# Performance work log

Hardware: AMD Instinct MI355X
Metric: run time of the kernel (lower is better)

The kernel has to match this reference:

```python
import jax, jax.numpy as jnp
import numpy as np

N, Q, CC = 8, 300, 92          # batch, queries, logit channels (91 classes + 1 objectness)
CF, HF, WF = 2048, 42, 42      # backbone feature map
M, TOPK = 20, 5                # GT boxes per image, pseudo-unknown top-k
NUM_CLASSES = 91
L_CLS, L_IOU, L_L1 = 2.0, 2.0, 5.0
NEG = -1e11


def cxcywh_to_xyxy(bx):
    cx, cy, bw, bh = bx[..., 0], bx[..., 1], bx[..., 2], bx[..., 3]
    return jnp.stack([cx - bw / 2, cy - bh / 2, cx + bw / 2, cy + bh / 2], -1)


def setup_inputs() -> dict:
    key = jax.random.key(0)
    ks = jax.random.split(key, 6)
    h = w = 1333
    img_features = jax.random.normal(ks[0], (N, CF, HF, WF), jnp.float32)
    pred_logits = jax.random.normal(ks[1], (N, Q, CC), jnp.float32)
    pred_boxes = jax.random.uniform(ks[2], (N, Q, 4), jnp.float32, 0.05, 0.95)
    tgt_labels = jax.random.randint(ks[3], (N, M), 0, NUM_CLASSES - 1).astype(jnp.int32)
    u = jax.random.uniform(ks[4], (N, M, 4), jnp.float32)
    # GT boxes in pixel cxcywh (bbox_normalize divides by image size)
    tgt_boxes = jnp.stack([u[..., 0] * w, u[..., 1] * h,
                           u[..., 2] * 0.3 * w + 2.0, u[..., 3] * 0.3 * h + 2.0], -1)
    perm = jax.vmap(lambda k: jax.random.permutation(k, Q))(jax.random.split(ks[5], N))
    query_idx = perm[:, :M].astype(jnp.int32)          # unique matched query per target
    tgt_idx = jnp.tile(jnp.arange(M, dtype=jnp.int32), (N, 1))
    return dict(img_features=img_features, pred_logits=pred_logits, pred_boxes=pred_boxes,
                tgt_labels=tgt_labels, tgt_boxes=tgt_boxes, query_idx=query_idx,
                tgt_idx=tgt_idx, h=h, w=w)


def _loss(img_features, pred_logits, pred_boxes, tgt_boxes, tgt_labels, query_idx, tgt_idx, h, w):
    b = jnp.arange(N)[:, None]
    scale = jnp.array([w, h, w, h], jnp.float32)
    out_prob = jnp.concatenate([jax.nn.softmax(pred_logits[..., :-1], -1),
                                jax.nn.sigmoid(pred_logits[..., -1:])], -1)  # [N,Q,92]
    matched_mask = jnp.zeros((N, Q), bool).at[b, query_idx].set(True)

    # --- per-query crop-mean pooling: bilinear upsample once + summed-area table ---
    mean_feat = jnp.mean(img_features, 1)                                  # [N,HF,WF]
    up = jax.vmap(lambda f: jax.image.resize(f, (h, w), 'bilinear'))(mean_feat)  # [N,h,w]
    sat = jnp.pad(jnp.cumsum(jnp.cumsum(up, 1), 2), ((0, 0), (1, 0), (1, 0)))    # [N,h+1,w+1]
    bb = cxcywh_to_xyxy(pred_boxes) * scale                                # pixel xyxy
    x1 = jnp.clip(bb[..., 0].astype(jnp.int32), 0, w)
    y1 = jnp.clip(bb[..., 1].astype(jnp.int32), 0, h)
    x2 = jnp.clip(bb[..., 2].astype(jnp.int32), 0, w)
    y2 = jnp.clip(bb[..., 3].astype(jnp.int32), 0, h)
    cnt = jnp.maximum(y2 - y1, 0) * jnp.maximum(x2 - x1, 0)
    x2e, y2e = jnp.maximum(x2, x1), jnp.maximum(y2, y1)
    boxsum = sat[b, y2e, x2e] - sat[b, y1, x2e] - sat[b, y2e, x1] + sat[b, y1, x1]
    means = jnp.where(cnt > 0, boxsum / jnp.maximum(cnt, 1), NEG)          # empty crop -> -1e11 (nan case)
    means = jnp.where(matched_mask, NEG, means)                            # matched queries excluded
    _, topk_idx = jax.lax.top_k(means, TOPK)                               # [N,TOPK]
    topk_mask = jnp.zeros((N, Q), bool).at[b, topk_idx].set(True)

    # --- matched terms ---
    tgt_cls = tgt_labels[b, tgt_idx]                                       # [N,M]
    tgt_bb = tgt_boxes[b, tgt_idx] / scale                                 # bbox_normalize
    q_cls = out_prob[b, query_idx, :NUM_CLASSES]                           # probs; CE re-applies log_softmax (faithful)
    q_obj = out_prob[b, query_idx, -1]
    q_bb = pred_boxes[b, query_idx]
    logp = jax.nn.log_softmax(q_cls, -1)
    ce_matched = -jnp.mean(jnp.take_along_axis(logp, tgt_cls[..., None].astype(jnp.int32), -1)[..., 0], 1)
    bce_matched = -jnp.mean(jnp.maximum(jnp.log(q_obj), -100.0), 1)
    l1 = jnp.sqrt(jnp.sum((q_bb - tgt_bb) ** 2, (1, 2)))                   # torch.dist (Frobenius)
    a, t = cxcywh_to_xyxy(q_bb), cxcywh_to_xyxy(tgt_bb)
    ix1 = jnp.maximum(a[..., 0], t[..., 0]); iy1 = jnp.maximum(a[..., 1], t[..., 1])
    ix2 = jnp.minimum(a[..., 2], t[..., 2]); iy2 = jnp.minimum(a[..., 3], t[..., 3])
    inter = jnp.clip(ix2 - ix1, 0.0) * jnp.clip(iy2 - iy1, 0.0)
    area = lambda z: (z[..., 2] - z[..., 0]) * (z[..., 3] - z[..., 1])
    iou = inter / (area(a) + area(t) - inter + 1e-9)
    iou_loss = jnp.sum(1.0 - iou, 1)

    # --- pseudo-unknown terms ---
    pk_cls = out_prob[b, topk_idx, :NUM_CLASSES]
    ce_pseudo = -jnp.mean(jax.nn.log_softmax(pk_cls, -1)[..., NUM_CLASSES - 1], 1)
    pk_obj = out_prob[b, topk_idx, -1]
    bce_topk = -jnp.mean(jnp.maximum(jnp.log(pk_obj), -100.0), 1)
    rest = (~matched_mask) & (~topk_mask)                                  # setdiff(other, topk)
    neglog1m = -jnp.maximum(jnp.log1p(-out_prob[..., -1]), -100.0)
    bce_rest = jnp.sum(jnp.where(rest, neglog1m, 0.0), 1) / jnp.maximum(jnp.sum(rest, 1), 1)

    cls_loss = jnp.sum(ce_matched + ce_pseudo)
    obj_loss = jnp.sum(bce_matched + bce_rest + bce_topk)
    return (cls_loss * L_CLS + obj_loss * L_CLS
            + jnp.sum(iou_loss) * L_IOU + jnp.sum(l1) * L_L1)


def reference(img_features, pred_logits, pred_boxes, tgt_labels, tgt_boxes, query_idx, tgt_idx, h, w):
    return _loss(img_features, pred_logits, pred_boxes, tgt_boxes, tgt_labels, query_idx, tgt_idx, h, w)
```

## Files before the change

### kernel.cpp

```cpp
#include <hip/hip_runtime.h>
#include <math.h>

#define NB 8
#define QN 300
#define CCH 92
#define NCLS 91
#define CFCH 2048
#define HFD 42
#define MT 20
#define TOPK5 5
#define DIM 1333
#define DIMF 1333.0f
#define PIX (HFD*HFD)
#define PIX4 (PIX/4)
#define CHUNKS 64
#define CPC (CFCH/CHUNKS)
#define NEGV -100000000000.0f

#define PART_BLOCKS (NB*CHUNKS*2)
#define CUM_TOTAL   (2*(DIM+1)*HFD)
#define CUM_BLOCKS  ((CUM_TOTAL + 255)/256)

__device__ __forceinline__ float bilin_w(int i, int j, float s) {
    float sf = ((float)i + 0.5f) * s - 0.5f;
    if (sf <= 0.f)                return (j == 0) ? 1.f : 0.f;
    if (sf >= (float)(HFD - 1))   return (j == HFD - 1) ? 1.f : 0.f;
    int j0 = (int)sf;
    float fr = sf - (float)j0;
    if (j == j0)     return 1.f - fr;
    if (j == j0 + 1) return fr;
    return 0.f;
}

__device__ __forceinline__ float wave_sum(float v) {
    for (int off = 32; off; off >>= 1) v += __shfl_down(v, off);
    return v;
}

__global__ __launch_bounds__(256) void stage_a(const float4* __restrict__ img,
                                               float4* __restrict__ part,
                                               float* __restrict__ CX,
                                               float* __restrict__ CY,
                                               float* __restrict__ out) {
    int blk = blockIdx.x;
    if (blk == 0 && threadIdx.x == 0) out[0] = 0.f;
    if (blk < PART_BLOCKS) {
        int tile = blk & 1;
        int chunk = (blk >> 1) & (CHUNKS - 1);
        int b = blk >> 7;
        int f = tile * 256 + threadIdx.x;
        if (f >= PIX4) return;
        const float4* p = img + (size_t)(b * CFCH + chunk * CPC) * PIX4 + f;
        float x = 0.f, y = 0.f, z = 0.f, w = 0.f;
#pragma unroll 8
        for (int k = 0; k < CPC; ++k) {
            float4 v = p[(size_t)k * PIX4];
            x += v.x; y += v.y; z += v.z; w += v.w;
        }
        float4 o; o.x = x; o.y = y; o.z = z; o.w = w;
        part[(size_t)(blk >> 1) * PIX4 + f] = o;
    } else {
        int idx = (blk - PART_BLOCKS) * 256 + threadIdx.x;
        const int total = (DIM + 1) * HFD;
        int t = idx / total;
        if (t >= 2) return;
        int rem = idx - t * total;
        int X = rem / HFD;
        int j = rem - X * HFD;
        const float s = (float)HFD / DIMF;
        int i0 = max(0, (int)floorf(((float)j - 0.5f) / s - 0.5f) - 2);
        int i1 = min(DIM, (int)ceilf(((float)j + 1.5f) / s - 0.5f) + 2);
        int hi = min(X, i1);
        float acc = 0.f;
        for (int i = i0; i < hi; ++i) acc += bilin_w(i, j, s);
        float* C = t ? CY : CX;
        C[X * HFD + j] = acc;
    }
}

__global__ __launch_bounds__(256) void chan_reduce(const float* __restrict__ part,
                                                   float* __restrict__ mf) {
    int idx = blockIdx.x * 256 + threadIdx.x;
    if (idx >= NB * PIX) return;
    int b = idx / PIX, pix = idx - b * PIX;
    const float* pp = part + (size_t)b * CHUNKS * PIX + pix;
    float acc = 0.f;
#pragma unroll 8
    for (int c = 0; c < CHUNKS; ++c) acc += pp[(size_t)c * PIX];
    mf[idx] = acc * (1.0f / (float)CFCH);
}

__global__ __launch_bounds__(256) void query_stats(
        const float* __restrict__ boxes, const int* __restrict__ query_idx,
        const int* __restrict__ tgt_idx, const int* __restrict__ tgt_labels,
        const float* __restrict__ tgt_boxes, const float* __restrict__ mf,
        const float* __restrict__ CX, const float* __restrict__ CY,
        const float* __restrict__ logits,
        float* __restrict__ means, float* __restrict__ ls2a,
        float* __restrict__ p90a, float* __restrict__ ptga,
        float* __restrict__ nobja, float* __restrict__ n1ma,
        float* __restrict__ l1a, float* __restrict__ ioua) {
    int gw = (blockIdx.x * 256 + threadIdx.x) >> 6;
    int lane = threadIdx.x & 63;
    if (gw >= NB * QN) return;
    int b = gw / QN, q = gw - b * QN;

    int mpos = -1;
#pragma unroll
    for (int m = 0; m < MT; ++m) if (query_idx[b * MT + m] == q) mpos = m;

    const float* bx = boxes + (size_t)gw * 4;
    float cx = bx[0], cy = bx[1], bw = bx[2], bh = bx[3];
    int x1 = min(max((int)((cx - bw * 0.5f) * DIMF), 0), DIM);
    int y1 = min(max((int)((cy - bh * 0.5f) * DIMF), 0), DIM);
    int x2 = min(max((int)((cx + bw * 0.5f) * DIMF), 0), DIM);
    int y2 = min(max((int)((cy + bh * 0.5f) * DIMF), 0), DIM);
    int x2e = max(x2, x1), y2e = max(y2, y1);
    int cnt = max(y2 - y1, 0) * max(x2 - x1, 0);
    float val = NEGV;
    if (mpos < 0 && cnt > 0) {
        float dxl = 0.f, dyl = 0.f;
        if (lane < HFD) {
            dxl = CX[x2e * HFD + lane] - CX[x1 * HFD + lane];
            dyl = CY[y2e * HFD + lane] - CY[y1 * HFD + lane];
        }
        float tacc = 0.f;
        if (lane < HFD) {
            const float* mb = mf + (size_t)b * PIX + lane;
            float inner = 0.f;
#pragma unroll 7
            for (int p = 0; p < HFD; ++p)
                inner += __shfl(dyl, p) * mb[p * HFD];
            tacc = dxl * inner;
        }
        tacc = wave_sum(tacc);
        val = tacc / (float)cnt;
    }

    const float* L = logits + (size_t)gw * CCH;
    float c0 = L[lane];
    float e1 = (lane < CCH - 64) ? L[lane + 64] : 0.f;
    bool has_c1 = (lane < NCLS - 64);
    float mx = fmaxf(c0, has_c1 ? e1 : -3.4e38f);
    for (int off = 32; off; off >>= 1) mx = fmaxf(mx, __shfl_xor(mx, off));
    float se = expf(c0 - mx) + (has_c1 ? expf(e1 - mx) : 0.f);
    for (int off = 32; off; off >>= 1) se += __shfl_xor(se, off);
    float inv = 1.f / se;
    float s2 = expf(expf(c0 - mx) * inv) + (has_c1 ? expf(expf(e1 - mx) * inv) : 0.f);
    for (int off = 32; off; off >>= 1) s2 += __shfl_xor(s2, off);
    float ls2 = logf(s2);
    float l90  = __shfl(e1, 26);
    float lobj = __shfl(e1, 27);
    float p90 = expf(l90 - mx) * inv;
    float sg = 1.f / (1.f + expf(-lobj));
    float nobj = -fmaxf(logf(sg), -100.f);
    float n1m  = -fmaxf(log1pf(-sg), -100.f);

    float ptg = 0.f, l1 = 0.f, iouc = 0.f;
    if (mpos >= 0) {
        int ti = tgt_idx[b * MT + mpos];
        int tc = tgt_labels[b * MT + ti];
        ptg = expf(L[tc] - mx) * inv;
        const float* tb = tgt_boxes + (size_t)(b * MT + ti) * 4;
        float t0 = tb[0] / DIMF, t1 = tb[1] / DIMF, t2 = tb[2] / DIMF, t3 = tb[3] / DIMF;
        float d0 = cx - t0, d1 = cy - t1, d2 = bw - t2, d3 = bh - t3;
        l1 = d0 * d0 + d1 * d1 + d2 * d2 + d3 * d3;
        float ax1 = cx - bw * 0.5f, ay1 = cy - bh * 0.5f;
        float ax2 = cx + bw * 0.5f, ay2 = cy + bh * 0.5f;
        float tx1 = t0 - t2 * 0.5f, ty1 = t1 - t3 * 0.5f;
        float tx2 = t0 + t2 * 0.5f, ty2 = t1 + t3 * 0.5f;
        float ix1 = fmaxf(ax1, tx1), iy1 = fmaxf(ay1, ty1);
        float ix2 = fminf(ax2, tx2), iy2 = fminf(ay2, ty2);
        float inter = fmaxf(ix2 - ix1, 0.f) * fmaxf(iy2 - iy1, 0.f);
        float aa = (ax2 - ax1) * (ay2 - ay1), at = (tx2 - tx1) * (ty2 - ty1);
        float iou = inter / (aa + at - inter + 1e-9f);
        iouc = 1.f - iou;
    }
    if (lane == 0) {
        means[gw] = val; ls2a[gw] = ls2; p90a[gw] = p90; ptga[gw] = ptg;
        nobja[gw] = nobj; n1ma[gw] = n1m; l1a[gw] = l1; ioua[gw] = iouc;
    }
}

__global__ __launch_bounds__(256) void finalize(
        const int* __restrict__ query_idx,
        const float* __restrict__ means, const float* __restrict__ ls2a,
        const float* __restrict__ p90a, const float* __restrict__ ptga,
        const float* __restrict__ nobja, const float* __restrict__ n1ma,
        const float* __restrict__ l1a, const float* __restrict__ ioua,
        float* __restrict__ out) {
    int b = blockIdx.x, tid = threadIdx.x;
    int wid = tid >> 6, lane = tid & 63;
    __shared__ float s_means[QN];
    __shared__ unsigned char s_matched[QN], s_sel[QN];
    __shared__ float s_red[4];
    __shared__ int s_redi[4];
    __shared__ float s_acc[4][8];

    for (int q = tid; q < QN; q += 256) {
        s_means[q] = means[b * QN + q];
        s_matched[q] = 0; s_sel[q] = 0;
    }
    __syncthreads();
    if (tid < MT) s_matched[query_idx[b * MT + tid]] = 1;
    __syncthreads();

    for (int r = 0; r < TOPK5; ++r) {
        float bv = -3.4e38f; int bi = QN;
        for (int q = tid; q < QN; q += 256) {
            if (!s_sel[q]) {
                float v = s_means[q];
                if (v > bv || (v == bv && q < bi)) { bv = v; bi = q; }
            }
        }
        for (int off = 32; off; off >>= 1) {
            float ov = __shfl_down(bv, off); int oi = __shfl_down(bi, off);
            if (ov > bv || (ov == bv && oi < bi)) { bv = ov; bi = oi; }
        }
        if (lane == 0) { s_red[wid] = bv; s_redi[wid] = bi; }
        __syncthreads();
        if (tid == 0) {
            float fv = s_red[0]; int fi = s_redi[0];
            for (int k = 1; k < 4; ++k)
                if (s_red[k] > fv || (s_red[k] == fv && s_redi[k] < fi)) { fv = s_red[k]; fi = s_redi[k]; }
            s_sel[fi] = 1;
        }
        __syncthreads();
    }

    float a0 = 0, a1 = 0, a2 = 0, a3 = 0, a4 = 0, a5 = 0, a6 = 0; int rc = 0;
    for (int q = tid; q < QN; q += 256) {
        int g = b * QN + q;
        if (s_matched[q]) {
            a0 += ls2a[g] - ptga[g];
            a1 += nobja[g];
            a2 += l1a[g];
            a3 += ioua[g];
        } else if (s_sel[q]) {
            a4 += ls2a[g] - p90a[g];
            a5 += nobja[g];
        } else {
            a6 += n1ma[g]; rc++;
        }
    }
    a0 = wave_sum(a0); a1 = wave_sum(a1); a2 = wave_sum(a2); a3 = wave_sum(a3);
    a4 = wave_sum(a4); a5 = wave_sum(a5); a6 = wave_sum(a6);
    float rcf = wave_sum((float)rc);
    if (lane == 0) {
        s_acc[wid][0] = a0; s_acc[wid][1] = a1; s_acc[wid][2] = a2; s_acc[wid][3] = a3;
        s_acc[wid][4] = a4; s_acc[wid][5] = a5; s_acc[wid][6] = a6; s_acc[wid][7] = rcf;
    }
    __syncthreads();
    if (tid == 0) {
        float A[8];
        for (int k = 0; k < 8; ++k)
            A[k] = s_acc[0][k] + s_acc[1][k] + s_acc[2][k] + s_acc[3][k];
        float ce_matched = A[0] / (float)MT;
        float bce_matched = A[1] / (float)MT;
        float l1 = sqrtf(A[2]);
        float iou_loss = A[3];
        float ce_pseudo = A[4] / (float)TOPK5;
        float bce_topk = A[5] / (float)TOPK5;
        int rcT = (int)(A[7] + 0.5f);
        float bce_rest = A[6] / (float)max(rcT, 1);
        float total = 2.f * (ce_matched + ce_pseudo)
                    + 2.f * (bce_matched + bce_rest + bce_topk)
                    + 2.f * iou_loss + 5.f * l1;
        atomicAdd(out, total);
    }
}

extern "C" void kernel_launch(void* const* d_in, const int* in_sizes, int n_in,
                              void* d_out, int out_size, void* d_ws, size_t ws_size,
                              hipStream_t stream) {
    const float* img        = (const float*)d_in[0];
    const float* logits     = (const float*)d_in[1];
    const float* boxes      = (const float*)d_in[2];
    const int*   tgt_labels = (const int*)d_in[3];
    const float* tgt_boxes  = (const float*)d_in[4];
    const int*   query_idx  = (const int*)d_in[5];
    const int*   tgt_idx    = (const int*)d_in[6];

    float* ws    = (float*)d_ws;
    float* part  = ws;
    float* mf    = part + (size_t)NB * CHUNKS * PIX;
    float* CX    = mf + (size_t)NB * PIX;
    float* CY    = CX + (size_t)(DIM + 1) * HFD;
    float* means = CY + (size_t)(DIM + 1) * HFD;
    float* ls2a  = means + NB * QN;
    float* p90a  = ls2a + NB * QN;
    float* ptga  = p90a + NB * QN;
    float* nobja = ptga + NB * QN;
    float* n1ma  = nobja + NB * QN;
    float* l1a   = n1ma + NB * QN;
    float* ioua  = l1a + NB * QN;

    stage_a<<<PART_BLOCKS + CUM_BLOCKS, 256, 0, stream>>>(
        (const float4*)img, (float4*)part, CX, CY, (float*)d_out);
    chan_reduce<<<(NB * PIX + 255) / 256, 256, 0, stream>>>(part, mf);
    query_stats<<<(NB * QN) / 4, 256, 0, stream>>>(
        boxes, query_idx, tgt_idx, tgt_labels, tgt_boxes, mf, CX, CY, logits,
        means, ls2a, p90a, ptga, nobja, n1ma, l1a, ioua);
    finalize<<<NB, 256, 0, stream>>>(query_idx, means, ls2a, p90a, ptga,
                                     nobja, n1ma, l1a, ioua, (float*)d_out);
}
```

Baseline: 202.9 us.

## Fuse channel reduction into query_stats and finalize in a single block

Removes the chan_reduce kernel. Each query_stats block now sums the per-chunk partials for its batch image into shared memory before doing the crop-mean dot products. Chunks are halved to 32, so stage_a does more channels per thread over fewer blocks. finalize now runs as one block that loops over all images and writes the output directly, dropping the zero-init and the atomic. The cost is that every query_stats block redundantly re-reduces the partial map for its image, 600 blocks each reading about 225 KB, and stage_a has less parallelism.

```diff
diff --git a/kernel.cpp b/kernel.cpp
--- a/kernel.cpp
+++ b/kernel.cpp
@@ -13,13 +13,14 @@
 #define DIMF 1333.0f
 #define PIX (HFD*HFD)
 #define PIX4 (PIX/4)
-#define CHUNKS 64
+#define CHUNKS 32
 #define CPC (CFCH/CHUNKS)
 #define NEGV -100000000000.0f
 
 #define PART_BLOCKS (NB*CHUNKS*2)
 #define CUM_TOTAL   (2*(DIM+1)*HFD)
 #define CUM_BLOCKS  ((CUM_TOTAL + 255)/256)
+#define QS_BLOCKS   ((NB*QN)/4)
 
 __device__ __forceinline__ float bilin_w(int i, int j, float s) {
     float sf = ((float)i + 0.5f) * s - 0.5f;
@@ -40,14 +41,12 @@
 __global__ __launch_bounds__(256) void stage_a(const float4* __restrict__ img,
                                                float4* __restrict__ part,
                                                float* __restrict__ CX,
-                                               float* __restrict__ CY,
-                                               float* __restrict__ out) {
+                                               float* __restrict__ CY) {
     int blk = blockIdx.x;
-    if (blk == 0 && threadIdx.x == 0) out[0] = 0.f;
     if (blk < PART_BLOCKS) {
         int tile = blk & 1;
         int chunk = (blk >> 1) & (CHUNKS - 1);
-        int b = blk >> 7;
+        int b = blk >> 6;
         int f = tile * 256 + threadIdx.x;
         if (f >= PIX4) return;
         const float4* p = img + (size_t)(b * CFCH + chunk * CPC) * PIX4 + f;
@@ -78,22 +77,11 @@
     }
 }
 
-__global__ __launch_bounds__(256) void chan_reduce(const float* __restrict__ part,
-                                                   float* __restrict__ mf) {
-    int idx = blockIdx.x * 256 + threadIdx.x;
-    if (idx >= NB * PIX) return;
-    int b = idx / PIX, pix = idx - b * PIX;
-    const float* pp = part + (size_t)b * CHUNKS * PIX + pix;
-    float acc = 0.f;
-#pragma unroll 8
-    for (int c = 0; c < CHUNKS; ++c) acc += pp[(size_t)c * PIX];
-    mf[idx] = acc * (1.0f / (float)CFCH);
-}
-
 __global__ __launch_bounds__(256) void query_stats(
+        const float4* __restrict__ part,
         const float* __restrict__ boxes, const int* __restrict__ query_idx,
         const int* __restrict__ tgt_idx, const int* __restrict__ tgt_labels,
-        const float* __restrict__ tgt_boxes, const float* __restrict__ mf,
+        const float* __restrict__ tgt_boxes,
         const float* __restrict__ CX, const float* __restrict__ CY,
         const float* __restrict__ logits,
         float* __restrict__ means, float* __restrict__ ls2a,
@@ -102,8 +90,26 @@
         float* __restrict__ l1a, float* __restrict__ ioua) {
     int gw = (blockIdx.x * 256 + threadIdx.x) >> 6;
     int lane = threadIdx.x & 63;
-    if (gw >= NB * QN) return;
     int b = gw / QN, q = gw - b * QN;
+
+    __shared__ float s_mf[PIX];
+    {
+        const float inv_cf = 1.0f / (float)CFCH;
+        const float4* pb = part + (size_t)b * CHUNKS * PIX4;
+        for (int f = threadIdx.x; f < PIX4; f += 256) {
+            float x = 0.f, y = 0.f, z = 0.f, w = 0.f;
+#pragma unroll 8
+            for (int c = 0; c < CHUNKS; ++c) {
+                float4 v = pb[(size_t)c * PIX4 + f];
+                x += v.x; y += v.y; z += v.z; w += v.w;
+            }
+            s_mf[4 * f + 0] = x * inv_cf;
+            s_mf[4 * f + 1] = y * inv_cf;
+            s_mf[4 * f + 2] = z * inv_cf;
+            s_mf[4 * f + 3] = w * inv_cf;
+        }
+    }
+    __syncthreads();
 
     int mpos = -1;
 #pragma unroll
@@ -126,11 +132,10 @@
         }
         float tacc = 0.f;
         if (lane < HFD) {
-            const float* mb = mf + (size_t)b * PIX + lane;
             float inner = 0.f;
 #pragma unroll 7
             for (int p = 0; p < HFD; ++p)
-                inner += __shfl(dyl, p) * mb[p * HFD];
+                inner += __shfl(dyl, p) * s_mf[p * HFD + lane];
             tacc = dxl * inner;
         }
         tacc = wave_sum(tacc);
@@ -189,7 +194,7 @@
         const float* __restrict__ nobja, const float* __restrict__ n1ma,
         const float* __restrict__ l1a, const float* __restrict__ ioua,
         float* __restrict__ out) {
-    int b = blockIdx.x, tid = threadIdx.x;
+    int tid = threadIdx.x;
     int wid = tid >> 6, lane = tid & 63;
     __shared__ float s_means[QN];
     __shared__ unsigned char s_matched[QN], s_sel[QN];
@@ -197,77 +202,81 @@
     __shared__ int s_redi[4];
     __shared__ float s_acc[4][8];
 
-    for (int q = tid; q < QN; q += 256) {
-        s_means[q] = means[b * QN + q];
-        s_matched[q] = 0; s_sel[q] = 0;
-    }
-    __syncthreads();
-    if (tid < MT) s_matched[query_idx[b * MT + tid]] = 1;
-    __syncthreads();
-
-    for (int r = 0; r < TOPK5; ++r) {
-        float bv = -3.4e38f; int bi = QN;
+    float grand = 0.f;
+    for (int b = 0; b < NB; ++b) {
         for (int q = tid; q < QN; q += 256) {
-            if (!s_sel[q]) {
-                float v = s_means[q];
-                if (v > bv || (v == bv && q < bi)) { bv = v; bi = q; }
-            }
-        }
-        for (int off = 32; off; off >>= 1) {
-            float ov = __shfl_down(bv, off); int oi = __shfl_down(bi, off);
-            if (ov > bv || (ov == bv && oi < bi)) { bv = ov; bi = oi; }
-        }
-        if (lane == 0) { s_red[wid] = bv; s_redi[wid] = bi; }
+            s_means[q] = means[b * QN + q];
+            s_matched[q] = 0; s_sel[q] = 0;
+        }
+        __syncthreads();
+        if (tid < MT) s_matched[query_idx[b * MT + tid]] = 1;
+        __syncthreads();
+
+        for (int r = 0; r < TOPK5; ++r) {
+            float bv = -3.4e38f; int bi = QN;
+            for (int q = tid; q < QN; q += 256) {
+                if (!s_sel[q]) {
+                    float v = s_means[q];
+                    if (v > bv || (v == bv && q < bi)) { bv = v; bi = q; }
+                }
+            }
+            for (int off = 32; off; off >>= 1) {
+                float ov = __shfl_down(bv, off); int oi = __shfl_down(bi, off);
+                if (ov > bv || (ov == bv && oi < bi)) { bv = ov; bi = oi; }
+            }
+            if (lane == 0) { s_red[wid] = bv; s_redi[wid] = bi; }
+            __syncthreads();
+            if (tid == 0) {
+                float fv = s_red[0]; int fi = s_redi[0];
+                for (int k = 1; k < 4; ++k)
+                    if (s_red[k] > fv || (s_red[k] == fv && s_redi[k] < fi)) { fv = s_red[k]; fi = s_redi[k]; }
+                s_sel[fi] = 1;
+            }
+            __syncthreads();
+        }
+
+        float a0 = 0, a1 = 0, a2 = 0, a3 = 0, a4 = 0, a5 = 0, a6 = 0; int rc = 0;
+        for (int q = tid; q < QN; q += 256) {
+            int g = b * QN + q;
+            if (s_matched[q]) {
+                a0 += ls2a[g] - ptga[g];
+                a1 += nobja[g];
+                a2 += l1a[g];
+                a3 += ioua[g];
+            } else if (s_sel[q]) {
+                a4 += ls2a[g] - p90a[g];
+                a5 += nobja[g];
+            } else {
+                a6 += n1ma[g]; rc++;
+            }
+        }
+        a0 = wave_sum(a0); a1 = wave_sum(a1); a2 = wave_sum(a2); a3 = wave_sum(a3);
+        a4 = wave_sum(a4); a5 = wave_sum(a5); a6 = wave_sum(a6);
+        float rcf = wave_sum((float)rc);
+        if (lane == 0) {
+            s_acc[wid][0] = a0; s_acc[wid][1] = a1; s_acc[wid][2] = a2; s_acc[wid][3] = a3;
+            s_acc[wid][4] = a4; s_acc[wid][5] = a5; s_acc[wid][6] = a6; s_acc[wid][7] = rcf;
+        }
         __syncthreads();
         if (tid == 0) {
-            float fv = s_red[0]; int fi = s_redi[0];
-            for (int k = 1; k < 4; ++k)
-                if (s_red[k] > fv || (s_red[k] == fv && s_redi[k] < fi)) { fv = s_red[k]; fi = s_redi[k]; }
-            s_sel[fi] = 1;
+            float A[8];
+            for (int k = 0; k < 8; ++k)
+                A[k] = s_acc[0][k] + s_acc[1][k] + s_acc[2][k] + s_acc[3][k];
+            float ce_matched = A[0] / (float)MT;
+            float bce_matched = A[1] / (float)MT;
+            float l1 = sqrtf(A[2]);
+            float iou_loss = A[3];
+            float ce_pseudo = A[4] / (float)TOPK5;
+            float bce_topk = A[5] / (float)TOPK5;
+            int rcT = (int)(A[7] + 0.5f);
+            float bce_rest = A[6] / (float)max(rcT, 1);
+            grand += 2.f * (ce_matched + ce_pseudo)
+                   + 2.f * (bce_matched + bce_rest + bce_topk)
+                   + 2.f * iou_loss + 5.f * l1;
         }
         __syncthreads();
     }
-
-    float a0 = 0, a1 = 0, a2 = 0, a3 = 0, a4 = 0, a5 = 0, a6 = 0; int rc = 0;
-    for (int q = tid; q < QN; q += 256) {
-        int g = b * QN + q;
-        if (s_matched[q]) {
-            a0 += ls2a[g] - ptga[g];
-            a1 += nobja[g];
-            a2 += l1a[g];
-            a3 += ioua[g];
-        } else if (s_sel[q]) {
-            a4 += ls2a[g] - p90a[g];
-            a5 += nobja[g];
-        } else {
-            a6 += n1ma[g]; rc++;
-        }
-    }
-    a0 = wave_sum(a0); a1 = wave_sum(a1); a2 = wave_sum(a2); a3 = wave_sum(a3);
-    a4 = wave_sum(a4); a5 = wave_sum(a5); a6 = wave_sum(a6);
-    float rcf = wave_sum((float)rc);
-    if (lane == 0) {
-        s_acc[wid][0] = a0; s_acc[wid][1] = a1; s_acc[wid][2] = a2; s_acc[wid][3] = a3;
-        s_acc[wid][4] = a4; s_acc[wid][5] = a5; s_acc[wid][6] = a6; s_acc[wid][7] = rcf;
-    }
-    __syncthreads();
-    if (tid == 0) {
-        float A[8];
-        for (int k = 0; k < 8; ++k)
-            A[k] = s_acc[0][k] + s_acc[1][k] + s_acc[2][k] + s_acc[3][k];
-        float ce_matched = A[0] / (float)MT;
-        float bce_matched = A[1] / (float)MT;
-        float l1 = sqrtf(A[2]);
-        float iou_loss = A[3];
-        float ce_pseudo = A[4] / (float)TOPK5;
-        float bce_topk = A[5] / (float)TOPK5;
-        int rcT = (int)(A[7] + 0.5f);
-        float bce_rest = A[6] / (float)max(rcT, 1);
-        float total = 2.f * (ce_matched + ce_pseudo)
-                    + 2.f * (bce_matched + bce_rest + bce_topk)
-                    + 2.f * iou_loss + 5.f * l1;
-        atomicAdd(out, total);
-    }
+    if (tid == 0) out[0] = grand;
 }
 
 extern "C" void kernel_launch(void* const* d_in, const int* in_sizes, int n_in,
@@ -283,8 +292,7 @@
 
     float* ws    = (float*)d_ws;
     float* part  = ws;
-    float* mf    = part + (size_t)NB * CHUNKS * PIX;
-    float* CX    = mf + (size_t)NB * PIX;
+    float* CX    = part + (size_t)NB * CHUNKS * PIX;
     float* CY    = CX + (size_t)(DIM + 1) * HFD;
     float* means = CY + (size_t)(DIM + 1) * HFD;
     float* ls2a  = means + NB * QN;
@@ -296,11 +304,10 @@
     float* ioua  = l1a + NB * QN;
 
     stage_a<<<PART_BLOCKS + CUM_BLOCKS, 256, 0, stream>>>(
-        (const float4*)img, (float4*)part, CX, CY, (float*)d_out);
-    chan_reduce<<<(NB * PIX + 255) / 256, 256, 0, stream>>>(part, mf);
-    query_stats<<<(NB * QN) / 4, 256, 0, stream>>>(
-        boxes, query_idx, tgt_idx, tgt_labels, tgt_boxes, mf, CX, CY, logits,
-        means, ls2a, p90a, ptga, nobja, n1ma, l1a, ioua);
-    finalize<<<NB, 256, 0, stream>>>(query_idx, means, ls2a, p90a, ptga,
-                                     nobja, n1ma, l1a, ioua, (float*)d_out);
-}
+        (const float4*)img, (float4*)part, CX, CY);
+    query_stats<<<QS_BLOCKS, 256, 0, stream>>>(
+        (const float4*)part, boxes, query_idx, tgt_idx, tgt_labels, tgt_boxes,
+        CX, CY, logits, means, ls2a, p90a, ptga, nobja, n1ma, l1a, ioua);
+    finalize<<<1, 256, 0, stream>>>(query_idx, means, ls2a, p90a, ptga,
+                                    nobja, n1ma, l1a, ioua, (float*)d_out);
+}
```

New measurement: 266.7 us. 1.31x slower.

## Move logit stats into stage_a and compute box means from LDS-staged features

Applied to the files above, without the earlier changes.

The per-query softmax, objectness, L1 and IoU statistics move out of the query kernel and run as extra blocks of the first kernel, so they overlap with the channel-reduction streaming. The remaining box_means kernel stages each image's mean feature map and the per-query interpolation weight differences in shared memory. It then does a direct weighted sum over pixels instead of a shuffle-based separable product. The channel chunk count is also halved, which means fewer partial sums and a cheaper chan_reduce, but fewer blocks each doing more loads in stage_a.

```diff
diff --git a/kernel.cpp b/kernel.cpp
--- a/kernel.cpp
+++ b/kernel.cpp
@@ -13,13 +13,15 @@
 #define DIMF 1333.0f
 #define PIX (HFD*HFD)
 #define PIX4 (PIX/4)
-#define CHUNKS 64
+#define CHUNKS 32
 #define CPC (CFCH/CHUNKS)
 #define NEGV -100000000000.0f
 
 #define PART_BLOCKS (NB*CHUNKS*2)
 #define CUM_TOTAL   (2*(DIM+1)*HFD)
 #define CUM_BLOCKS  ((CUM_TOTAL + 255)/256)
+#define STAT_BLOCKS ((NB*QN)/4)
+#define BM_BLOCKS   ((NB*QN)/4)
 
 __device__ __forceinline__ float bilin_w(int i, int j, float s) {
     float sf = ((float)i + 0.5f) * s - 0.5f;
@@ -37,17 +39,22 @@
     return v;
 }
 
-__global__ __launch_bounds__(256) void stage_a(const float4* __restrict__ img,
-                                               float4* __restrict__ part,
-                                               float* __restrict__ CX,
-                                               float* __restrict__ CY,
-                                               float* __restrict__ out) {
+__global__ __launch_bounds__(256) void stage_a(
+        const float4* __restrict__ img, float4* __restrict__ part,
+        float* __restrict__ CX, float* __restrict__ CY,
+        const float* __restrict__ logits, const float* __restrict__ boxes,
+        const int* __restrict__ query_idx, const int* __restrict__ tgt_idx,
+        const int* __restrict__ tgt_labels, const float* __restrict__ tgt_boxes,
+        float* __restrict__ ls2a, float* __restrict__ p90a,
+        float* __restrict__ ptga, float* __restrict__ nobja,
+        float* __restrict__ n1ma, float* __restrict__ l1a,
+        float* __restrict__ ioua, float* __restrict__ out) {
     int blk = blockIdx.x;
     if (blk == 0 && threadIdx.x == 0) out[0] = 0.f;
     if (blk < PART_BLOCKS) {
         int tile = blk & 1;
         int chunk = (blk >> 1) & (CHUNKS - 1);
-        int b = blk >> 7;
+        int b = blk >> 6;
         int f = tile * 256 + threadIdx.x;
         if (f >= PIX4) return;
         const float4* p = img + (size_t)(b * CFCH + chunk * CPC) * PIX4 + f;
@@ -59,7 +66,7 @@
         }
         float4 o; o.x = x; o.y = y; o.z = z; o.w = w;
         part[(size_t)(blk >> 1) * PIX4 + f] = o;
-    } else {
+    } else if (blk < PART_BLOCKS + CUM_BLOCKS) {
         int idx = (blk - PART_BLOCKS) * 256 + threadIdx.x;
         const int total = (DIM + 1) * HFD;
         int t = idx / total;
@@ -75,6 +82,58 @@
         for (int i = i0; i < hi; ++i) acc += bilin_w(i, j, s);
         float* C = t ? CY : CX;
         C[X * HFD + j] = acc;
+    } else {
+        int gw = (blk - PART_BLOCKS - CUM_BLOCKS) * 4 + (threadIdx.x >> 6);
+        int lane = threadIdx.x & 63;
+        int b = gw / QN, q = gw - b * QN;
+        int mpos = -1;
+#pragma unroll
+        for (int m = 0; m < MT; ++m) if (query_idx[b * MT + m] == q) mpos = m;
+        const float* L = logits + (size_t)gw * CCH;
+        float c0 = L[lane];
+        float e1 = (lane < CCH - 64) ? L[lane + 64] : 0.f;
+        bool has_c1 = (lane < NCLS - 64);
+        float mx = fmaxf(c0, has_c1 ? e1 : -3.4e38f);
+        for (int off = 32; off; off >>= 1) mx = fmaxf(mx, __shfl_xor(mx, off));
+        float se = expf(c0 - mx) + (has_c1 ? expf(e1 - mx) : 0.f);
+        for (int off = 32; off; off >>= 1) se += __shfl_xor(se, off);
+        float inv = 1.f / se;
+        float s2 = expf(expf(c0 - mx) * inv) + (has_c1 ? expf(expf(e1 - mx) * inv) : 0.f);
+        for (int off = 32; off; off >>= 1) s2 += __shfl_xor(s2, off);
+        float ls2 = logf(s2);
+        float l90  = __shfl(e1, 26);
+        float lobj = __shfl(e1, 27);
+        float p90 = expf(l90 - mx) * inv;
+        float sg = 1.f / (1.f + expf(-lobj));
+        float nobj = -fmaxf(logf(sg), -100.f);
+        float n1m  = -fmaxf(log1pf(-sg), -100.f);
+
+        float ptg = 0.f, l1 = 0.f, iouc = 0.f;
+        if (mpos >= 0) {
+            const float* bx = boxes + (size_t)gw * 4;
+            float cx = bx[0], cy = bx[1], bw = bx[2], bh = bx[3];
+            int ti = tgt_idx[b * MT + mpos];
+            int tc = tgt_labels[b * MT + ti];
+            ptg = expf(L[tc] - mx) * inv;
+            const float* tb = tgt_boxes + (size_t)(b * MT + ti) * 4;
+            float t0 = tb[0] / DIMF, t1 = tb[1] / DIMF, t2 = tb[2] / DIMF, t3 = tb[3] / DIMF;
+            float d0 = cx - t0, d1 = cy - t1, d2 = bw - t2, d3 = bh - t3;
+            l1 = d0 * d0 + d1 * d1 + d2 * d2 + d3 * d3;
+            float ax1 = cx - bw * 0.5f, ay1 = cy - bh * 0.5f;
+            float ax2 = cx + bw * 0.5f, ay2 = cy + bh * 0.5f;
+            float tx1 = t0 - t2 * 0.5f, ty1 = t1 - t3 * 0.5f;
+            float tx2 = t0 + t2 * 0.5f, ty2 = t1 + t3 * 0.5f;
+            float ix1 = fmaxf(ax1, tx1), iy1 = fmaxf(ay1, ty1);
+            float ix2 = fminf(ax2, tx2), iy2 = fminf(ay2, ty2);
+            float inter = fmaxf(ix2 - ix1, 0.f) * fmaxf(iy2 - iy1, 0.f);
+            float aa = (ax2 - ax1) * (ay2 - ay1), at = (tx2 - tx1) * (ty2 - ty1);
+            float iou = inter / (aa + at - inter + 1e-9f);
+            iouc = 1.f - iou;
+        }
+        if (lane == 0) {
+            ls2a[gw] = ls2; p90a[gw] = p90; ptga[gw] = ptg;
+            nobja[gw] = nobj; n1ma[gw] = n1m; l1a[gw] = l1; ioua[gw] = iouc;
+        }
     }
 }
 
@@ -90,20 +149,20 @@
     mf[idx] = acc * (1.0f / (float)CFCH);
 }
 
-__global__ __launch_bounds__(256) void query_stats(
-        const float* __restrict__ boxes, const int* __restrict__ query_idx,
-        const int* __restrict__ tgt_idx, const int* __restrict__ tgt_labels,
-        const float* __restrict__ tgt_boxes, const float* __restrict__ mf,
+__global__ __launch_bounds__(256) void box_means(
+        const float* __restrict__ mf, const float* __restrict__ boxes,
+        const int* __restrict__ query_idx,
         const float* __restrict__ CX, const float* __restrict__ CY,
-        const float* __restrict__ logits,
-        float* __restrict__ means, float* __restrict__ ls2a,
-        float* __restrict__ p90a, float* __restrict__ ptga,
-        float* __restrict__ nobja, float* __restrict__ n1ma,
-        float* __restrict__ l1a, float* __restrict__ ioua) {
-    int gw = (blockIdx.x * 256 + threadIdx.x) >> 6;
-    int lane = threadIdx.x & 63;
-    if (gw >= NB * QN) return;
+        float* __restrict__ means) {
+    int tid = threadIdx.x;
+    int gw = (blockIdx.x * 256 + tid) >> 6;
+    int lane = tid & 63, wid = tid >> 6;
     int b = gw / QN, q = gw - b * QN;
+
+    __shared__ float s_mf[PIX];
+    __shared__ float s_d[4][84];
+    for (int i = tid; i < PIX; i += 256) s_mf[i] = mf[b * PIX + i];
+    __syncthreads();
 
     int mpos = -1;
 #pragma unroll
@@ -117,69 +176,27 @@
     int y2 = min(max((int)((cy + bh * 0.5f) * DIMF), 0), DIM);
     int x2e = max(x2, x1), y2e = max(y2, y1);
     int cnt = max(y2 - y1, 0) * max(x2 - x1, 0);
+
     float val = NEGV;
     if (mpos < 0 && cnt > 0) {
-        float dxl = 0.f, dyl = 0.f;
         if (lane < HFD) {
-            dxl = CX[x2e * HFD + lane] - CX[x1 * HFD + lane];
-            dyl = CY[y2e * HFD + lane] - CY[y1 * HFD + lane];
-        }
-        float tacc = 0.f;
-        if (lane < HFD) {
-            const float* mb = mf + (size_t)b * PIX + lane;
-            float inner = 0.f;
-#pragma unroll 7
-            for (int p = 0; p < HFD; ++p)
-                inner += __shfl(dyl, p) * mb[p * HFD];
-            tacc = dxl * inner;
-        }
-        tacc = wave_sum(tacc);
-        val = tacc / (float)cnt;
-    }
-
-    const float* L = logits + (size_t)gw * CCH;
-    float c0 = L[lane];
-    float e1 = (lane < CCH - 64) ? L[lane + 64] : 0.f;
-    bool has_c1 = (lane < NCLS - 64);
-    float mx = fmaxf(c0, has_c1 ? e1 : -3.4e38f);
-    for (int off = 32; off; off >>= 1) mx = fmaxf(mx, __shfl_xor(mx, off));
-    float se = expf(c0 - mx) + (has_c1 ? expf(e1 - mx) : 0.f);
-    for (int off = 32; off; off >>= 1) se += __shfl_xor(se, off);
-    float inv = 1.f / se;
-    float s2 = expf(expf(c0 - mx) * inv) + (has_c1 ? expf(expf(e1 - mx) * inv) : 0.f);
-    for (int off = 32; off; off >>= 1) s2 += __shfl_xor(s2, off);
-    float ls2 = logf(s2);
-    float l90  = __shfl(e1, 26);
-    float lobj = __shfl(e1, 27);
-    float p90 = expf(l90 - mx) * inv;
-    float sg = 1.f / (1.f + expf(-lobj));
-    float nobj = -fmaxf(logf(sg), -100.f);
-    float n1m  = -fmaxf(log1pf(-sg), -100.f);
-
-    float ptg = 0.f, l1 = 0.f, iouc = 0.f;
-    if (mpos >= 0) {
-        int ti = tgt_idx[b * MT + mpos];
-        int tc = tgt_labels[b * MT + ti];
-        ptg = expf(L[tc] - mx) * inv;
-        const float* tb = tgt_boxes + (size_t)(b * MT + ti) * 4;
-        float t0 = tb[0] / DIMF, t1 = tb[1] / DIMF, t2 = tb[2] / DIMF, t3 = tb[3] / DIMF;
-        float d0 = cx - t0, d1 = cy - t1, d2 = bw - t2, d3 = bh - t3;
-        l1 = d0 * d0 + d1 * d1 + d2 * d2 + d3 * d3;
-        float ax1 = cx - bw * 0.5f, ay1 = cy - bh * 0.5f;
-        float ax2 = cx + bw * 0.5f, ay2 = cy + bh * 0.5f;
-        float tx1 = t0 - t2 * 0.5f, ty1 = t1 - t3 * 0.5f;
-        float tx2 = t0 + t2 * 0.5f, ty2 = t1 + t3 * 0.5f;
-        float ix1 = fmaxf(ax1, tx1), iy1 = fmaxf(ay1, ty1);
-        float ix2 = fminf(ax2, tx2), iy2 = fminf(ay2, ty2);
-        float inter = fmaxf(ix2 - ix1, 0.f) * fmaxf(iy2 - iy1, 0.f);
-        float aa = (ax2 - ax1) * (ay2 - ay1), at = (tx2 - tx1) * (ty2 - ty1);
-        float iou = inter / (aa + at - inter + 1e-9f);
-        iouc = 1.f - iou;
-    }
-    if (lane == 0) {
-        means[gw] = val; ls2a[gw] = ls2; p90a[gw] = p90; ptga[gw] = ptg;
-        nobja[gw] = nobj; n1ma[gw] = n1m; l1a[gw] = l1; ioua[gw] = iouc;
-    }
+            s_d[wid][lane]      = CY[y2e * HFD + lane] - CY[y1 * HFD + lane];
+            s_d[wid][42 + lane] = CX[x2e * HFD + lane] - CX[x1 * HFD + lane];
+        }
+        float acc = 0.f;
+#pragma unroll
+        for (int i = 0; i < 28; ++i) {
+            int pix = lane + (i << 6);
+            if (pix < PIX) {
+                int row = pix / HFD;
+                int col = pix - row * HFD;
+                acc += s_d[wid][row] * s_d[wid][42 + col] * s_mf[pix];
+            }
+        }
+        acc = wave_sum(acc);
+        val = acc / (float)cnt;
+    }
+    if (lane == 0) means[gw] = val;
 }
 
 __global__ __launch_bounds__(256) void finalize(
@@ -295,12 +312,12 @@
     float* l1a   = n1ma + NB * QN;
     float* ioua  = l1a + NB * QN;
 
-    stage_a<<<PART_BLOCKS + CUM_BLOCKS, 256, 0, stream>>>(
-        (const float4*)img, (float4*)part, CX, CY, (float*)d_out);
+    stage_a<<<PART_BLOCKS + CUM_BLOCKS + STAT_BLOCKS, 256, 0, stream>>>(
+        (const float4*)img, (float4*)part, CX, CY, logits, boxes,
+        query_idx, tgt_idx, tgt_labels, tgt_boxes,
+        ls2a, p90a, ptga, nobja, n1ma, l1a, ioua, (float*)d_out);
     chan_reduce<<<(NB * PIX + 255) / 256, 256, 0, stream>>>(part, mf);
-    query_stats<<<(NB * QN) / 4, 256, 0, stream>>>(
-        boxes, query_idx, tgt_idx, tgt_labels, tgt_boxes, mf, CX, CY, logits,
-        means, ls2a, p90a, ptga, nobja, n1ma, l1a, ioua);
+    box_means<<<BM_BLOCKS, 256, 0, stream>>>(mf, boxes, query_idx, CX, CY, means);
     finalize<<<NB, 256, 0, stream>>>(query_idx, means, ls2a, p90a, ptga,
                                      nobja, n1ma, l1a, ioua, (float*)d_out);
 }
```

Measured after the change: 202.8 us. Within noise of the previous version (-0.1%).
